# Performance work log

Hardware: AMD Instinct MI355X
Metric: run time of the kernel (lower is better)

The kernel has to match this reference:

```python
import jax, jax.numpy as jnp
import numpy as np

N = 50000      # nodes in batched graph
E = 800000     # directed edges
F_IN = 64      # node_feature_dim
F_E = 16       # edge_feature_dim
H = 4          # heads
C = 64         # hidden_dim per head
HC = H * C     # 256


def setup_inputs() -> dict:
    key = jax.random.key(0)
    ks = jax.random.split(key, 26)
    rn = lambda k, s, scale=0.1: jax.random.normal(k, s, dtype=jnp.float32) * scale
    inp = {}
    inp["x"] = rn(ks[0], (N, F_IN), 1.0)
    inp["edge_src"] = jax.random.randint(ks[1], (E,), 0, N)
    inp["edge_dst"] = jax.random.randint(ks[2], (E,), 0, N)
    inp["edge_attr"] = rn(ks[3], (E, F_E), 1.0)
    # GATConv layer 1 params
    inp["W1"] = rn(ks[4], (F_IN, HC))
    inp["atts1"] = rn(ks[5], (H, C))
    inp["attd1"] = rn(ks[6], (H, C))
    inp["We1"] = rn(ks[7], (F_E, HC))
    inp["atte1"] = rn(ks[8], (H, C))
    inp["b1"] = jnp.zeros((HC,), jnp.float32)
    inp["g1"] = jnp.ones((HC,), jnp.float32)
    inp["be1"] = jnp.zeros((HC,), jnp.float32)
    # GATConv layer 2 params
    inp["W2"] = rn(ks[9], (HC, HC))
    inp["atts2"] = rn(ks[10], (H, C))
    inp["attd2"] = rn(ks[11], (H, C))
    inp["We2"] = rn(ks[12], (F_E, HC))
    inp["atte2"] = rn(ks[13], (H, C))
    inp["b2"] = jnp.zeros((HC,), jnp.float32)
    inp["g2"] = jnp.ones((HC,), jnp.float32)
    inp["be2"] = jnp.zeros((HC,), jnp.float32)
    # output head
    inp["Wout"] = rn(ks[14], (HC, 1))
    inp["bout"] = jnp.zeros((1,), jnp.float32)
    return inp


def _gat_layer(x, src, dst, eattr, W, att_s, att_d, We, att_e, b):
    """PyG GATConv (concat=True, add_self_loops with fill_value='mean', eval so no dropout)."""
    n = x.shape[0]
    e = src.shape[0]
    # self-loop edge attr = mean of incoming edge attrs per node (0 if none)
    deg = jax.ops.segment_sum(jnp.ones((e,), x.dtype), dst, num_segments=n)
    loop_attr = jax.ops.segment_sum(eattr, dst, num_segments=n) / jnp.maximum(deg, 1.0)[:, None]
    loop = jnp.arange(n)
    src2 = jnp.concatenate([src, loop])
    dst2 = jnp.concatenate([dst, loop])
    ea2 = jnp.concatenate([eattr, loop_attr], axis=0)
    xs = (x @ W).reshape(n, H, C)                          # [N,H,C]
    a_s = jnp.einsum('nhc,hc->nh', xs, att_s)              # [N,H]
    a_d = jnp.einsum('nhc,hc->nh', xs, att_d)
    ee = (ea2 @ We).reshape(-1, H, C)                      # [E+N,H,C]
    a_e = jnp.einsum('ehc,hc->eh', ee, att_e)
    logits = jax.nn.leaky_relu(a_s[src2] + a_d[dst2] + a_e, 0.2)  # [E+N,H]
    m = jax.ops.segment_max(logits, dst2, num_segments=n)
    p = jnp.exp(logits - m[dst2])
    denom = jax.ops.segment_sum(p, dst2, num_segments=n)[dst2] + 1e-16
    alpha = p / denom                                      # segment softmax per dst node
    out = jax.ops.segment_sum(xs[src2] * alpha[:, :, None], dst2, num_segments=n)
    return out.reshape(n, HC) + b


def _bn_relu(x, g, b):
    # BatchNorm1d in training mode (batch statistics), eps=1e-5
    mu = x.mean(axis=0)
    var = ((x - mu) ** 2).mean(axis=0)
    return jax.nn.relu(g * (x - mu) * jax.lax.rsqrt(var + 1e-5) + b)


def reference(x, edge_src, edge_dst, edge_attr,
              W1, atts1, attd1, We1, atte1, b1, g1, be1,
              W2, atts2, attd2, We2, atte2, b2, g2, be2,
              Wout, bout):
    h = _gat_layer(x, edge_src, edge_dst, edge_attr, W1, atts1, attd1, We1, atte1, b1)
    h = _bn_relu(h, g1, be1)
    h = _gat_layer(h, edge_src, edge_dst, edge_attr, W2, atts2, attd2, We2, atte2, b2)
    h = _bn_relu(h, g2, be2)
    return h @ Wout + bout
```

## Files before the change

kernel.cpp:

```cpp
#include <hip/hip_runtime.h>
#include <hip/hip_bf16.h>
#include <stdint.h>

#define NNODES 50000
#define NEDGES 800000
#define HC 256

typedef unsigned short u16;
typedef __attribute__((ext_vector_type(8))) short bf16x8;
typedef __attribute__((ext_vector_type(4))) float f32x4;

__device__ __forceinline__ float b2f(u16 v) {
    return __uint_as_float(((unsigned)v) << 16);
}
__device__ __forceinline__ u16 f2b(float f) {
    unsigned u = __float_as_uint(f);
    u += 0x7fff + ((u >> 16) & 1);
    return (u16)(u >> 16);
}

__device__ __constant__ int dPO[19] = {0,16384,16640,16896,20992,21248,21504,21760,22016,
                                       87552,87808,88064,92160,92416,92672,92928,93184,93440,93441};
static const int hPO[19] = {0,16384,16640,16896,20992,21248,21504,21760,22016,
                            87552,87808,88064,92160,92416,92672,92928,93184,93440,93441};
#define TOTP 93441

__global__ void zero_init(unsigned* __restrict__ p, long nwords) {
    long i = (long)blockIdx.x * blockDim.x + threadIdx.x;
    long stride = (long)gridDim.x * blockDim.x;
    for (; i < nwords; i += stride) p[i] = 0u;
}

__global__ void detect_dtype(const unsigned* __restrict__ xbits, int* __restrict__ flag) {
    __shared__ int cnt;
    if (threadIdx.x == 0) cnt = 0;
    __syncthreads();
    int sane = 0;
    for (int i = threadIdx.x; i < 1024; i += 256) {
        unsigned lo = xbits[i] & 0xffffu;
        int e = (int)((lo >> 7) & 0xff);
        if (e >= 117 && e <= 133) sane++;
    }
    atomicAdd(&cnt, sane);
    __syncthreads();
    if (threadIdx.x == 0) *flag = (cnt >= 512) ? 1 : 0;
}

__global__ void cvt_bf16(const void* __restrict__ src, u16* __restrict__ dst, int n,
                         const int* __restrict__ flag) {
    int isbf16 = *flag;
    int i = blockIdx.x * 256 + threadIdx.x;
    int stride = gridDim.x * 256;
    if (isbf16) {
        const u16* s = (const u16*)src;
        for (; i < n; i += stride) dst[i] = s[i];
    } else {
        const float* s = (const float*)src;
        for (; i < n; i += stride) dst[i] = f2b(s[i]);
    }
}

struct Ptrs18 { const void* s[18]; };
__global__ void cvt_params(Ptrs18 p, u16* __restrict__ dst, const int* __restrict__ flag) {
    int i = blockIdx.x * 256 + threadIdx.x;
    if (i >= TOTP) return;
    int isbf16 = *flag;
    int idx = 0;
    #pragma unroll
    for (int j = 1; j < 18; j++) idx += (i >= dPO[j]) ? 1 : 0;
    int rel = i - dPO[idx];
    dst[i] = isbf16 ? ((const u16*)p.s[idx])[rel] : f2b(((const float*)p.s[idx])[rel]);
}

__global__ void proj_weight(const u16* __restrict__ W, const u16* __restrict__ att,
                            float* __restrict__ out, int R) {
    int i = blockIdx.x * 256 + threadIdx.x;
    if (i >= R * 4) return;
    int f = i >> 2, h = i & 3;
    float s = 0.f;
    for (int c = 0; c < 64; c++)
        s += b2f(W[f * 256 + h * 64 + c]) * b2f(att[h * 64 + c]);
    out[i] = s;
}

__global__ void proj_weight2(const u16* __restrict__ W, const u16* __restrict__ atta,
                             const u16* __restrict__ attb,
                             float* __restrict__ outa, float* __restrict__ outb, int R) {
    int i = blockIdx.x * 256 + threadIdx.x;
    if (i >= R * 4) return;
    int f = i >> 2, h = i & 3;
    float sa = 0.f, sb = 0.f;
    for (int c = 0; c < 64; c++) {
        float w = b2f(W[f * 256 + h * 64 + c]);
        sa += w * b2f(atta[h * 64 + c]);
        sb += w * b2f(attb[h * 64 + c]);
    }
    outa[i] = sa;
    outb[i] = sb;
}

__global__ void transpose_w(const u16* __restrict__ W, u16* __restrict__ WT, int K) {
    int i = blockIdx.x * 256 + threadIdx.x;
    if (i >= K * 256) return;
    int k = i / 256, c = i % 256;
    WT[c * K + k] = W[i];
}

__global__ void edge_deg(const int* __restrict__ edst, int* __restrict__ deg) {
    int e = blockIdx.x * 256 + threadIdx.x;
    if (e >= NEDGES) return;
    atomicAdd(&deg[edst[e]], 1);
}

__global__ void block_sum(const int* __restrict__ deg, int* __restrict__ bsums, int n) {
    __shared__ int lds[256];
    int i = blockIdx.x * 256 + threadIdx.x;
    lds[threadIdx.x] = (i < n) ? deg[i] : 0;
    __syncthreads();
    for (int s = 128; s; s >>= 1) {
        if (threadIdx.x < s) lds[threadIdx.x] += lds[threadIdx.x + s];
        __syncthreads();
    }
    if (threadIdx.x == 0) bsums[blockIdx.x] = lds[0];
}

__global__ void scan_bsums(const int* __restrict__ bsums, int* __restrict__ boffs, int nb) {
    __shared__ int lds[256];
    int t = threadIdx.x;
    int v = (t < nb) ? bsums[t] : 0;
    lds[t] = v;
    __syncthreads();
    for (int s = 1; s < 256; s <<= 1) {
        int u = (t >= s) ? lds[t - s] : 0;
        __syncthreads();
        lds[t] += u;
        __syncthreads();
    }
    boffs[t] = lds[t] - v;
}

__global__ void write_offsets(const int* __restrict__ deg, const int* __restrict__ boffs,
                              int* __restrict__ off, int* __restrict__ cursor, int n) {
    __shared__ int lds[256];
    int t = threadIdx.x;
    int i = blockIdx.x * 256 + t;
    int v = (i < n) ? deg[i] : 0;
    lds[t] = v;
    __syncthreads();
    for (int s = 1; s < 256; s <<= 1) {
        int u = (t >= s) ? lds[t - s] : 0;
        __syncthreads();
        lds[t] += u;
        __syncthreads();
    }
    int exc = lds[t] - v + boffs[blockIdx.x];
    if (i < n) { off[i] = exc; cursor[i] = exc; }
}

__global__ __launch_bounds__(256) void edge_stage(
    const void* __restrict__ eattr_raw, const int* __restrict__ flag,
    const int* __restrict__ esrc, const int* __restrict__ edst,
    const float* __restrict__ ve1, const float* __restrict__ ve2,
    int* __restrict__ cursor, uint4* __restrict__ rec) {
    int e = blockIdx.x * 256 + threadIdx.x;
    if (e >= NEDGES) return;
    float a[16];
    if (*flag) {
        const u16* s = (const u16*)eattr_raw + (long)e * 16;
        const uint4* q = (const uint4*)s;
        uint4 q0 = q[0], q1 = q[1];
        unsigned w0[8] = {q0.x, q0.y, q0.z, q0.w, q1.x, q1.y, q1.z, q1.w};
        #pragma unroll
        for (int j = 0; j < 8; j++) {
            a[2 * j] = b2f((u16)(w0[j] & 0xffff));
            a[2 * j + 1] = b2f((u16)(w0[j] >> 16));
        }
    } else {
        const float* s = (const float*)eattr_raw + (long)e * 16;
        #pragma unroll
        for (int j = 0; j < 16; j += 4) {
            float4 q = *(const float4*)(s + j);
            a[j] = q.x; a[j + 1] = q.y; a[j + 2] = q.z; a[j + 3] = q.w;
        }
    }
    float s1[4], s2[4];
    #pragma unroll
    for (int h = 0; h < 4; h++) {
        float t1 = 0.f, t2 = 0.f;
        #pragma unroll
        for (int f = 0; f < 16; f++) {
            t1 += a[f] * ve1[f * 4 + h];
            t2 += a[f] * ve2[f * 4 + h];
        }
        s1[h] = t1;
        s2[h] = t2;
    }
    unsigned a1lo = (unsigned)f2b(s1[0]) | ((unsigned)f2b(s1[1]) << 16);
    unsigned a1hi = (unsigned)f2b(s1[2]) | ((unsigned)f2b(s1[3]) << 16);
    unsigned a2lo = (unsigned)f2b(s2[0]) | ((unsigned)f2b(s2[1]) << 16);
    unsigned a2hi = (unsigned)f2b(s2[2]) | ((unsigned)f2b(s2[3]) << 16);
    int d = edst[e];
    int p = atomicAdd(&cursor[d], 1);
    unsigned src = (unsigned)esrc[e];
    rec[(long)p * 2 + 0] = make_uint4(src, a1lo, a1hi, 0u);
    rec[(long)p * 2 + 1] = make_uint4(src, a2lo, a2hi, 0u);
}

__global__ void bn_coef(const float* __restrict__ stats, const u16* __restrict__ g,
                        const u16* __restrict__ be, float* __restrict__ coef) {
    int c = threadIdx.x;
    float mu = stats[c] * (1.0f / NNODES);
    float var = stats[256 + c] * (1.0f / NNODES) - mu * mu;
    var = fmaxf(var, 0.f);
    float rs = rsqrtf(var + 1e-5f);
    float sc = b2f(g[c]) * rs;
    coef[c] = sc;
    coef[256 + c] = b2f(be[c]) - sc * mu;
}

template <int K, bool BN>
__global__ __launch_bounds__(256) void gemm_mfma(const u16* __restrict__ A,
                                                 const u16* __restrict__ WT,
                                                 const float* __restrict__ coef,
                                                 u16* __restrict__ out) {
    int tid = threadIdx.x;
    int wave = tid >> 6, lane = tid & 63;
    int quad = lane >> 4, l15 = lane & 15;
    long row0 = (long)blockIdx.x * 16;
    const u16* Arow = A + (row0 + l15) * K + quad * 8;
    const u16* Wbase = WT + (long)(wave * 64 + l15) * K + quad * 8;
    f32x4 acc[4] = {};
    for (int kk = 0; kk < K; kk += 32) {
        bf16x8 av = *(const bf16x8*)(Arow + kk);
        if (BN) {
            int kb = kk + quad * 8;
            float4 sc0 = *(const float4*)(coef + kb);
            float4 sc1 = *(const float4*)(coef + kb + 4);
            float4 sh0 = *(const float4*)(coef + 256 + kb);
            float4 sh1 = *(const float4*)(coef + 256 + kb + 4);
            float scl[8] = {sc0.x, sc0.y, sc0.z, sc0.w, sc1.x, sc1.y, sc1.z, sc1.w};
            float shf[8] = {sh0.x, sh0.y, sh0.z, sh0.w, sh1.x, sh1.y, sh1.z, sh1.w};
            #pragma unroll
            for (int j = 0; j < 8; j++) {
                float v = b2f((u16)av[j]);
                v = fmaxf(v * scl[j] + shf[j], 0.f);
                av[j] = (short)f2b(v);
            }
        }
        #pragma unroll
        for (int nt = 0; nt < 4; nt++) {
            bf16x8 bv = *(const bf16x8*)(Wbase + (long)nt * 16 * K + kk);
            acc[nt] = __builtin_amdgcn_mfma_f32_16x16x32_bf16(av, bv, acc[nt], 0, 0, 0);
        }
    }
    u16* orow = out + row0 * HC;
    #pragma unroll
    for (int nt = 0; nt < 4; nt++) {
        #pragma unroll
        for (int j = 0; j < 4; j++) {
            int r = quad * 4 + j;
            int c = wave * 64 + nt * 16 + l15;
            orow[(long)r * HC + c] = f2b(acc[nt][j]);
        }
    }
}

template <int K, bool BN>
__global__ __launch_bounds__(256) void proj_att(const u16* __restrict__ X,
                                                const float* __restrict__ coef,
                                                const float* __restrict__ us,
                                                const float* __restrict__ ud,
                                                float* __restrict__ as_, float* __restrict__ ad_) {
    int wid = (blockIdx.x * 256 + threadIdx.x) >> 6;
    int lane = threadIdx.x & 63;
    if (wid >= NNODES) return;
    float pas[4] = {0.f, 0.f, 0.f, 0.f}, pad[4] = {0.f, 0.f, 0.f, 0.f};
    const u16* row = X + (long)wid * K;
    for (int f = lane; f < K; f += 64) {
        float xv = b2f(row[f]);
        if (BN) xv = fmaxf(xv * coef[f] + coef[256 + f], 0.f);
        #pragma unroll
        for (int h = 0; h < 4; h++) {
            pas[h] += xv * us[f * 4 + h];
            pad[h] += xv * ud[f * 4 + h];
        }
    }
    #pragma unroll
    for (int h = 0; h < 4; h++) {
        for (int o = 32; o; o >>= 1) {
            pas[h] += __shfl_down(pas[h], o);
            pad[h] += __shfl_down(pad[h], o);
        }
    }
    if (lane == 0) {
        #pragma unroll
        for (int h = 0; h < 4; h++) {
            as_[wid * 4 + h] = pas[h];
            ad_[wid * 4 + h] = pad[h];
        }
    }
}

__global__ __launch_bounds__(256) void gat_fused(
    const u16* __restrict__ xs, const float* __restrict__ as_, const float* __restrict__ ad_,
    const uint4* __restrict__ rec, int layer,
    const int* __restrict__ off, const int* __restrict__ deg,
    const u16* __restrict__ bias, u16* __restrict__ out) {
    __shared__ int s_lds[4][64];
    __shared__ float w_lds[4][64][4];
    int wid = (blockIdx.x * 256 + threadIdx.x) >> 6;
    if (wid >= NNODES) return;
    int wave = threadIdx.x >> 6;
    int lane = threadIdx.x & 63;
    int d = wid;
    int st = off[d], dg = deg[d];
    int slot = lane >> 2, h = lane & 3;
    float adv = ad_[d * 4 + h];
    float m = -1e30f, s = 0.f, sae = 0.f;
    const uint4* rbase = rec + (long)st * 2 + layer;

    if (dg <= 64) {
        for (int i = slot; i < dg; i += 16) {
            uint4 r4 = rbase[(long)i * 2];
            int src = (int)r4.x;
            unsigned wsel = (h & 2) ? r4.z : r4.y;
            float aev = b2f((u16)((h & 1) ? (wsel >> 16) : (wsel & 0xffffu)));
            float t = as_[src * 4 + h] + adv + aev;
            float lg = (t > 0.f) ? t : 0.2f * t;
            if (h == 0) s_lds[wave][i] = src;
            w_lds[wave][i][h] = lg;
            sae += aev;
            float mn = fmaxf(m, lg);
            s = s * __expf(m - mn) + __expf(lg - mn);
            m = mn;
        }
        #pragma unroll
        for (int o = 4; o < 64; o <<= 1) {
            float mo = __shfl_xor(m, o), so = __shfl_xor(s, o), ao = __shfl_xor(sae, o);
            float mn = fmaxf(m, mo);
            s = s * __expf(m - mn) + so * __expf(mo - mn);
            m = mn;
            sae += ao;
        }
        float invs, wself;
        {
            float asv = as_[d * 4 + h];
            float l0 = asv + adv + sae / fmaxf((float)dg, 1.f);
            l0 = (l0 > 0.f) ? l0 : 0.2f * l0;
            float mn = fmaxf(m, l0);
            s = s * __expf(m - mn) + __expf(l0 - mn);
            m = mn;
            invs = 1.f / s;
            wself = __expf(l0 - mn) * invs;
        }
        for (int i = slot; i < dg; i += 16)
            w_lds[wave][i][h] = __expf(w_lds[wave][i][h] - m) * invs;

        int cg = lane & 31, half = lane >> 5;
        int ch8 = cg * 8;
        int h2 = cg >> 3;
        float ws2 = __shfl(wself, h2);
        const u16* xbase = xs + ch8;
        float a0, a1, a2, a3, a4, a5, a6, a7;
        {
            uint4 v = *(const uint4*)(xbase + (long)d * HC);
            float wsf = half ? 0.f : ws2;
            a0 = wsf * b2f((u16)(v.x & 0xffffu)); a1 = wsf * b2f((u16)(v.x >> 16));
            a2 = wsf * b2f((u16)(v.y & 0xffffu)); a3 = wsf * b2f((u16)(v.y >> 16));
            a4 = wsf * b2f((u16)(v.z & 0xffffu)); a5 = wsf * b2f((u16)(v.z >> 16));
            a6 = wsf * b2f((u16)(v.w & 0xffffu)); a7 = wsf * b2f((u16)(v.w >> 16));
        }
        int i = half;
        for (; i + 6 < dg; i += 8) {
            float wA = w_lds[wave][i][h2];     int sA = s_lds[wave][i];
            float wB = w_lds[wave][i + 2][h2]; int sB = s_lds[wave][i + 2];
            float wC = w_lds[wave][i + 4][h2]; int sC = s_lds[wave][i + 4];
            float wD = w_lds[wave][i + 6][h2]; int sD = s_lds[wave][i + 6];
            uint4 vA = *(const uint4*)(xbase + (long)sA * HC);
            uint4 vB = *(const uint4*)(xbase + (long)sB * HC);
            uint4 vC = *(const uint4*)(xbase + (long)sC * HC);
            uint4 vD = *(const uint4*)(xbase + (long)sD * HC);
            a0 += wA * b2f((u16)(vA.x & 0xffffu)) + wB * b2f((u16)(vB.x & 0xffffu))
                + wC * b2f((u16)(vC.x & 0xffffu)) + wD * b2f((u16)(vD.x & 0xffffu));
            a1 += wA * b2f((u16)(vA.x >> 16))     + wB * b2f((u16)(vB.x >> 16))
                + wC * b2f((u16)(vC.x >> 16))     + wD * b2f((u16)(vD.x >> 16));
            a2 += wA * b2f((u16)(vA.y & 0xffffu)) + wB * b2f((u16)(vB.y & 0xffffu))
                + wC * b2f((u16)(vC.y & 0xffffu)) + wD * b2f((u16)(vD.y & 0xffffu));
            a3 += wA * b2f((u16)(vA.y >> 16))     + wB * b2f((u16)(vB.y >> 16))
                + wC * b2f((u16)(vC.y >> 16))     + wD * b2f((u16)(vD.y >> 16));
            a4 += wA * b2f((u16)(vA.z & 0xffffu)) + wB * b2f((u16)(vB.z & 0xffffu))
                + wC * b2f((u16)(vC.z & 0xffffu)) + wD * b2f((u16)(vD.z & 0xffffu));
            a5 += wA * b2f((u16)(vA.z >> 16))     + wB * b2f((u16)(vB.z >> 16))
                + wC * b2f((u16)(vC.z >> 16))     + wD * b2f((u16)(vD.z >> 16));
            a6 += wA * b2f((u16)(vA.w & 0xffffu)) + wB * b2f((u16)(vB.w & 0xffffu))
                + wC * b2f((u16)(vC.w & 0xffffu)) + wD * b2f((u16)(vD.w & 0xffffu));
            a7 += wA * b2f((u16)(vA.w >> 16))     + wB * b2f((u16)(vB.w >> 16))
                + wC * b2f((u16)(vC.w >> 16))     + wD * b2f((u16)(vD.w >> 16));
        }
        for (; i < dg; i += 2) {
            float wA = w_lds[wave][i][h2]; int sA = s_lds[wave][i];
            uint4 vA = *(const uint4*)(xbase + (long)sA * HC);
            a0 += wA * b2f((u16)(vA.x & 0xffffu)); a1 += wA * b2f((u16)(vA.x >> 16));
            a2 += wA * b2f((u16)(vA.y & 0xffffu)); a3 += wA * b2f((u16)(vA.y >> 16));
            a4 += wA * b2f((u16)(vA.z & 0xffffu)); a5 += wA * b2f((u16)(vA.z >> 16));
            a6 += wA * b2f((u16)(vA.w & 0xffffu)); a7 += wA * b2f((u16)(vA.w >> 16));
        }
        a0 += __shfl_xor(a0, 32); a1 += __shfl_xor(a1, 32);
        a2 += __shfl_xor(a2, 32); a3 += __shfl_xor(a3, 32);
        a4 += __shfl_xor(a4, 32); a5 += __shfl_xor(a5, 32);
        a6 += __shfl_xor(a6, 32); a7 += __shfl_xor(a7, 32);
        if (half == 0) {
            uint4 bv = *(const uint4*)(bias + ch8);
            a0 += b2f((u16)(bv.x & 0xffffu)); a1 += b2f((u16)(bv.x >> 16));
            a2 += b2f((u16)(bv.y & 0xffffu)); a3 += b2f((u16)(bv.y >> 16));
            a4 += b2f((u16)(bv.z & 0xffffu)); a5 += b2f((u16)(bv.z >> 16));
            a6 += b2f((u16)(bv.w & 0xffffu)); a7 += b2f((u16)(bv.w >> 16));
            uint4 ov;
            ov.x = (unsigned)f2b(a0) | ((unsigned)f2b(a1) << 16);
            ov.y = (unsigned)f2b(a2) | ((unsigned)f2b(a3) << 16);
            ov.z = (unsigned)f2b(a4) | ((unsigned)f2b(a5) << 16);
            ov.w = (unsigned)f2b(a6) | ((unsigned)f2b(a7) << 16);
            *(uint4*)(out + (long)d * HC + ch8) = ov;
        }
        return;
    }

    for (int base = 0; base < dg; base += 16) {
        int i = base + slot;
        float lg = -1e30f, aev = 0.f, w = 0.f;
        if (i < dg) {
            uint4 r4 = rbase[(long)i * 2];
            int src = (int)r4.x;
            unsigned wsel = (h & 2) ? r4.z : r4.y;
            aev = b2f((u16)((h & 1) ? (wsel >> 16) : (wsel & 0xffffu)));
            float t = as_[src * 4 + h] + adv + aev;
            lg = (t > 0.f) ? t : 0.2f * t;
        }
        sae += aev;
        float mn = fmaxf(m, lg);
        if (i < dg) w = __expf(lg - mn);
        s = s * __expf(m - mn) + w;
        m = mn;
    }
    #pragma unroll
    for (int o = 4; o < 64; o <<= 1) {
        float mo = __shfl_xor(m, o), so = __shfl_xor(s, o), ao = __shfl_xor(sae, o);
        float mn = fmaxf(m, mo);
        s = s * __expf(m - mn) + so * __expf(mo - mn);
        m = mn;
        sae += ao;
    }
    float invs, wself;
    {
        float asv = as_[d * 4 + h];
        float l0 = asv + adv + sae / fmaxf((float)dg, 1.f);
        l0 = (l0 > 0.f) ? l0 : 0.2f * l0;
        float mn = fmaxf(m, l0);
        s = s * __expf(m - mn) + __expf(l0 - mn);
        m = mn;
        invs = 1.f / s;
        wself = __expf(l0 - mn) * invs;
    }
    int h2 = lane >> 4;
    float m2 = __shfl(m, h2);
    float is2 = __shfl(invs, h2);
    float ws2 = __shfl(wself, h2);
    float adv2 = __shfl(adv, h2);
    int cb = lane * 4;
    float a0, a1, a2, a3;
    {
        uint2 v = *(const uint2*)(xs + (long)d * HC + cb);
        a0 = ws2 * b2f((u16)(v.x & 0xffffu)); a1 = ws2 * b2f((u16)(v.x >> 16));
        a2 = ws2 * b2f((u16)(v.y & 0xffffu)); a3 = ws2 * b2f((u16)(v.y >> 16));
    }
    int slot16 = lane & 15;
    int lhi = lane & 48;
    for (int base = 0; base < dg; base += 16) {
        int cnt = min(16, dg - base);
        float wv = 0.f;
        int srcl = 0;
        if (slot16 < cnt) {
            uint4 r4 = rbase[(long)(base + slot16) * 2];
            srcl = (int)r4.x;
            unsigned wsel = (h2 & 2) ? r4.z : r4.y;
            float aev = b2f((u16)((h2 & 1) ? (wsel >> 16) : (wsel & 0xffffu)));
            float t = as_[srcl * 4 + h2] + adv2 + aev;
            t = (t > 0.f) ? t : 0.2f * t;
            wv = __expf(t - m2) * is2;
        }
        for (int j = 0; j < cnt; j++) {
            float w0 = __shfl(wv, lhi | j);
            int s0 = __shfl(srcl, j);
            uint2 v0 = *(const uint2*)(xs + (long)s0 * HC + cb);
            a0 += w0 * b2f((u16)(v0.x & 0xffffu));
            a1 += w0 * b2f((u16)(v0.x >> 16));
            a2 += w0 * b2f((u16)(v0.y & 0xffffu));
            a3 += w0 * b2f((u16)(v0.y >> 16));
        }
    }
    u16 o0 = f2b(a0 + b2f(bias[cb + 0]));
    u16 o1 = f2b(a1 + b2f(bias[cb + 1]));
    u16 o2 = f2b(a2 + b2f(bias[cb + 2]));
    u16 o3 = f2b(a3 + b2f(bias[cb + 3]));
    uint2 ov;
    ov.x = (unsigned)o0 | ((unsigned)o1 << 16);
    ov.y = (unsigned)o2 | ((unsigned)o3 << 16);
    *(uint2*)(out + (long)d * HC + cb) = ov;
}

__global__ void bn_stats(const u16* __restrict__ h, float* __restrict__ stats) {
    int c = threadIdx.x;
    float s = 0.f, q = 0.f;
    for (int r = blockIdx.x; r < NNODES; r += gridDim.x) {
        float v = b2f(h[(long)r * HC + c]);
        s += v;
        q += v * v;
    }
    atomicAdd(&stats[c], s);
    atomicAdd(&stats[256 + c], q);
}

__global__ __launch_bounds__(256) void out_head(const u16* __restrict__ h,
                                                const float* __restrict__ coef,
                                                const u16* __restrict__ wout,
                                                const u16* __restrict__ bout,
                                                void* __restrict__ y,
                                                const int* __restrict__ flag) {
    int wid = (blockIdx.x * 256 + threadIdx.x) >> 6;
    int lane = threadIdx.x & 63;
    if (wid >= NNODES) return;
    const u16* r = h + (long)wid * HC + lane * 4;
    int c0 = lane * 4;
    float p = 0.f;
    #pragma unroll
    for (int j = 0; j < 4; j++) {
        float v = b2f(r[j]);
        v = fmaxf(v * coef[c0 + j] + coef[256 + c0 + j], 0.f);
        p += v * b2f(wout[c0 + j]);
    }
    for (int o = 32; o; o >>= 1) p += __shfl_down(p, o);
    if (lane == 0) {
        float v = p + b2f(bout[0]);
        if (*flag) ((u16*)y)[wid] = f2b(v);
        else       ((float*)y)[wid] = v;
    }
}

extern "C" void kernel_launch(void* const* d_in, const int* in_sizes, int n_in,
                              void* d_out, int out_size, void* d_ws, size_t ws_size,
                              hipStream_t stream) {
    (void)in_sizes; (void)n_in; (void)out_size; (void)ws_size;
    const void* x_raw     = d_in[0];
    const int*  esrc      = (const int*)d_in[1];
    const int*  edst      = (const int*)d_in[2];
    const void* eattr_raw = d_in[3];

    char* ws = (char*)d_ws;
    size_t o = 0;
    auto alloc = [&](size_t bytes) -> char* {
        o = (o + 255) & ~(size_t)255;
        char* p = ws + o;
        o += bytes;
        return p;
    };
    int* dflag = (int*)alloc(256);
    u16* xb   = (u16*)alloc((size_t)NNODES * 64 * 2);
    u16* pall = (u16*)alloc((size_t)TOTP * 2);
    u16 *W1b = pall + hPO[0], *atts1b = pall + hPO[1], *attd1b = pall + hPO[2],
        *We1b = pall + hPO[3], *atte1b = pall + hPO[4], *b1b = pall + hPO[5],
        *g1b = pall + hPO[6], *be1b = pall + hPO[7], *W2b = pall + hPO[8],
        *atts2b = pall + hPO[9], *attd2b = pall + hPO[10], *We2b = pall + hPO[11],
        *atte2b = pall + hPO[12], *b2b = pall + hPO[13], *g2b = pall + hPO[14],
        *be2b = pall + hPO[15], *Woutb = pall + hPO[16], *boutb = pall + hPO[17];
    u16* WT1 = (u16*)alloc(256 * 64 * 2);
    u16* WT2 = (u16*)alloc(256 * 256 * 2);
    float* ve1 = (float*)alloc(64 * 4);
    float* ve2 = (float*)alloc(64 * 4);
    float* us1 = (float*)alloc(256 * 4);
    float* ud1 = (float*)alloc(256 * 4);
    float* us2 = (float*)alloc(1024 * 4);
    float* ud2 = (float*)alloc(1024 * 4);
    float* coef1 = (float*)alloc(512 * 4);
    float* coef2 = (float*)alloc(512 * 4);
    int* deg = (int*)alloc((size_t)NNODES * 4);
    float* stats1 = (float*)alloc(512 * 4);
    float* stats2 = (float*)alloc(512 * 4);
    size_t zero_end = o;
    size_t zero_begin = (size_t)((char*)deg - ws);
    int* off = (int*)alloc((size_t)NNODES * 4);
    int* cursor = (int*)alloc((size_t)NNODES * 4);
    int* bsums = (int*)alloc(256 * 4);
    int* boffs = (int*)alloc(256 * 4);
    uint4* rec = (uint4*)alloc((size_t)NEDGES * 32);
    float* as_ = (float*)alloc((size_t)NNODES * 16);
    float* ad_ = (float*)alloc((size_t)NNODES * 16);
    u16* bufA = (u16*)alloc((size_t)NNODES * HC * 2);
    u16* bufB = (u16*)alloc((size_t)NNODES * HC * 2);

    long zwords = (long)((zero_end - zero_begin) / 4);
    zero_init<<<128, 256, 0, stream>>>((unsigned*)(ws + zero_begin), zwords);
    detect_dtype<<<1, 256, 0, stream>>>((const unsigned*)x_raw, dflag);

    cvt_bf16<<<2048, 256, 0, stream>>>(x_raw, xb, NNODES * 64, dflag);
    Ptrs18 pp;
    for (int i = 0; i < 18; i++) pp.s[i] = d_in[4 + i];
    cvt_params<<<(TOTP + 255) / 256, 256, 0, stream>>>(pp, pall, dflag);

    transpose_w<<<64, 256, 0, stream>>>(W1b, WT1, 64);
    transpose_w<<<256, 256, 0, stream>>>(W2b, WT2, 256);
    proj_weight<<<1, 256, 0, stream>>>(We1b, atte1b, ve1, 16);
    proj_weight<<<1, 256, 0, stream>>>(We2b, atte2b, ve2, 16);
    proj_weight2<<<1, 256, 0, stream>>>(W1b, atts1b, attd1b, us1, ud1, 64);
    proj_weight2<<<4, 256, 0, stream>>>(W2b, atts2b, attd2b, us2, ud2, 256);

    int eblocks = (NEDGES + 255) / 256;
    int nb = (NNODES + 255) / 256;
    edge_deg<<<eblocks, 256, 0, stream>>>(edst, deg);
    block_sum<<<nb, 256, 0, stream>>>(deg, bsums, NNODES);
    scan_bsums<<<1, 256, 0, stream>>>(bsums, boffs, nb);
    write_offsets<<<nb, 256, 0, stream>>>(deg, boffs, off, cursor, NNODES);
    edge_stage<<<eblocks, 256, 0, stream>>>(eattr_raw, dflag, esrc, edst, ve1, ve2,
                                            cursor, rec);

    int mtiles = NNODES / 16;
    int wblocks = (NNODES * 64 + 255) / 256;

    gemm_mfma<64, false><<<mtiles, 256, 0, stream>>>(xb, WT1, nullptr, bufA);
    proj_att<64, false><<<wblocks, 256, 0, stream>>>(xb, nullptr, us1, ud1, as_, ad_);
    gat_fused<<<wblocks, 256, 0, stream>>>(bufA, as_, ad_, rec, 0, off, deg, b1b, bufB);
    bn_stats<<<512, 256, 0, stream>>>(bufB, stats1);
    bn_coef<<<1, 256, 0, stream>>>(stats1, g1b, be1b, coef1);

    gemm_mfma<256, true><<<mtiles, 256, 0, stream>>>(bufB, WT2, coef1, bufA);
    proj_att<256, true><<<wblocks, 256, 0, stream>>>(bufB, coef1, us2, ud2, as_, ad_);
    gat_fused<<<wblocks, 256, 0, stream>>>(bufA, as_, ad_, rec, 1, off, deg, b2b, bufB);
    bn_stats<<<512, 256, 0, stream>>>(bufB, stats2);
    bn_coef<<<1, 256, 0, stream>>>(stats2, g2b, be2b, coef2);

    out_head<<<wblocks, 256, 0, stream>>>(bufB, coef2, Woutb, boutb, d_out, dflag);
}
```

Baseline: 617.5 us.

## Use LDS-tiled 128x128 MFMA GEMM and split BN-ReLU into separate in-place pass

```diff
diff --git a/kernel.cpp b/kernel.cpp
--- a/kernel.cpp
+++ b/kernel.cpp
@@ -218,49 +218,89 @@
     coef[256 + c] = b2f(be[c]) - sc * mu;
 }
 
-template <int K, bool BN>
-__global__ __launch_bounds__(256) void gemm_mfma(const u16* __restrict__ A,
+__global__ __launch_bounds__(256) void bn_apply(u16* __restrict__ h,
+                                                const float* __restrict__ coef) {
+    long i = (long)blockIdx.x * 256 + threadIdx.x;
+    long total = (long)NNODES * (HC / 8);
+    long stride = (long)gridDim.x * 256;
+    int cpos = (int)(i & 31) * 8;
+    float scl[8], shf[8];
+    #pragma unroll
+    for (int j = 0; j < 8; j++) {
+        scl[j] = coef[cpos + j];
+        shf[j] = coef[256 + cpos + j];
+    }
+    for (; i < total; i += stride) {
+        uint4 v = *((const uint4*)h + i);
+        unsigned w[4] = {v.x, v.y, v.z, v.w};
+        #pragma unroll
+        for (int q = 0; q < 4; q++) {
+            float lo = b2f((u16)(w[q] & 0xffffu));
+            float hi = b2f((u16)(w[q] >> 16));
+            lo = fmaxf(lo * scl[2 * q] + shf[2 * q], 0.f);
+            hi = fmaxf(hi * scl[2 * q + 1] + shf[2 * q + 1], 0.f);
+            w[q] = (unsigned)f2b(lo) | ((unsigned)f2b(hi) << 16);
+        }
+        *((uint4*)h + i) = make_uint4(w[0], w[1], w[2], w[3]);
+    }
+}
+
+__device__ __forceinline__ void gload_lds16(const u16* g, u16* l) {
+    __builtin_amdgcn_global_load_lds(
+        (const __attribute__((address_space(1))) unsigned*)g,
+        (__attribute__((address_space(3))) unsigned*)l, 16, 0, 0);
+}
+
+template <int K>
+__global__ __launch_bounds__(256) void gemm_tile(const u16* __restrict__ A,
                                                  const u16* __restrict__ WT,
-                                                 const float* __restrict__ coef,
                                                  u16* __restrict__ out) {
+    __shared__ u16 As[128 * 32];
+    __shared__ u16 Bs[128 * 32];
     int tid = threadIdx.x;
     int wave = tid >> 6, lane = tid & 63;
+    int wr = wave >> 1, wc = wave & 1;
     int quad = lane >> 4, l15 = lane & 15;
-    long row0 = (long)blockIdx.x * 16;
-    const u16* Arow = A + (row0 + l15) * K + quad * 8;
-    const u16* Wbase = WT + (long)(wave * 64 + l15) * K + quad * 8;
-    f32x4 acc[4] = {};
+    long row0 = (long)(blockIdx.x >> 1) * 128;
+    int col0 = (blockIdx.x & 1) * 128;
+    int srow = lane >> 2;
+    int soct = (lane & 3) * 8;
+    f32x4 acc[4][4] = {};
     for (int kk = 0; kk < K; kk += 32) {
-        bf16x8 av = *(const bf16x8*)(Arow + kk);
-        if (BN) {
-            int kb = kk + quad * 8;
-            float4 sc0 = *(const float4*)(coef + kb);
-            float4 sc1 = *(const float4*)(coef + kb + 4);
-            float4 sh0 = *(const float4*)(coef + 256 + kb);
-            float4 sh1 = *(const float4*)(coef + 256 + kb + 4);
-            float scl[8] = {sc0.x, sc0.y, sc0.z, sc0.w, sc1.x, sc1.y, sc1.z, sc1.w};
-            float shf[8] = {sh0.x, sh0.y, sh0.z, sh0.w, sh1.x, sh1.y, sh1.z, sh1.w};
+        #pragma unroll
+        for (int sub = 0; sub < 2; sub++) {
+            int rr = wave * 32 + sub * 16;
+            long gr = row0 + rr + srow;
+            if (gr >= NNODES) gr = NNODES - 1;
+            gload_lds16(A + gr * K + kk + soct, &As[rr * 32]);
+            gload_lds16(WT + (long)(col0 + rr + srow) * K + kk + soct, &Bs[rr * 32]);
+        }
+        __syncthreads();
+        bf16x8 av[4], bv[4];
+        #pragma unroll
+        for (int m = 0; m < 4; m++)
+            av[m] = *(const bf16x8*)&As[(wr * 64 + m * 16 + l15) * 32 + quad * 8];
+        #pragma unroll
+        for (int n = 0; n < 4; n++)
+            bv[n] = *(const bf16x8*)&Bs[(wc * 64 + n * 16 + l15) * 32 + quad * 8];
+        #pragma unroll
+        for (int m = 0; m < 4; m++)
             #pragma unroll
-            for (int j = 0; j < 8; j++) {
-                float v = b2f((u16)av[j]);
-                v = fmaxf(v * scl[j] + shf[j], 0.f);
-                av[j] = (short)f2b(v);
+            for (int n = 0; n < 4; n++)
+                acc[m][n] = __builtin_amdgcn_mfma_f32_16x16x32_bf16(av[m], bv[n],
+                                                                    acc[m][n], 0, 0, 0);
+        __syncthreads();
+    }
+    #pragma unroll
+    for (int m = 0; m < 4; m++) {
+        #pragma unroll
+        for (int j = 0; j < 4; j++) {
+            long r = row0 + wr * 64 + m * 16 + quad * 4 + j;
+            if (r < NNODES) {
+                u16* op = out + r * HC + col0 + wc * 64 + l15;
+                #pragma unroll
+                for (int n = 0; n < 4; n++) op[n * 16] = f2b(acc[m][n][j]);
             }
-        }
-        #pragma unroll
-        for (int nt = 0; nt < 4; nt++) {
-            bf16x8 bv = *(const bf16x8*)(Wbase + (long)nt * 16 * K + kk);
-            acc[nt] = __builtin_amdgcn_mfma_f32_16x16x32_bf16(av, bv, acc[nt], 0, 0, 0);
-        }
-    }
-    u16* orow = out + row0 * HC;
-    #pragma unroll
-    for (int nt = 0; nt < 4; nt++) {
-        #pragma unroll
-        for (int j = 0; j < 4; j++) {
-            int r = quad * 4 + j;
-            int c = wave * 64 + nt * 16 + l15;
-            orow[(long)r * HC + c] = f2b(acc[nt][j]);
         }
     }
 }
@@ -622,17 +662,18 @@
     edge_stage<<<eblocks, 256, 0, stream>>>(eattr_raw, dflag, esrc, edst, ve1, ve2,
                                             cursor, rec);
 
-    int mtiles = NNODES / 16;
+    int gtiles = ((NNODES + 127) / 128) * 2;
     int wblocks = (NNODES * 64 + 255) / 256;
 
-    gemm_mfma<64, false><<<mtiles, 256, 0, stream>>>(xb, WT1, nullptr, bufA);
+    gemm_tile<64><<<gtiles, 256, 0, stream>>>(xb, WT1, bufA);
     proj_att<64, false><<<wblocks, 256, 0, stream>>>(xb, nullptr, us1, ud1, as_, ad_);
     gat_fused<<<wblocks, 256, 0, stream>>>(bufA, as_, ad_, rec, 0, off, deg, b1b, bufB);
     bn_stats<<<512, 256, 0, stream>>>(bufB, stats1);
     bn_coef<<<1, 256, 0, stream>>>(stats1, g1b, be1b, coef1);
 
-    gemm_mfma<256, true><<<mtiles, 256, 0, stream>>>(bufB, WT2, coef1, bufA);
-    proj_att<256, true><<<wblocks, 256, 0, stream>>>(bufB, coef1, us2, ud2, as_, ad_);
+    bn_apply<<<2048, 256, 0, stream>>>(bufB, coef1);
+    gemm_tile<256><<<gtiles, 256, 0, stream>>>(bufB, WT2, bufA);
+    proj_att<256, false><<<wblocks, 256, 0, stream>>>(bufB, nullptr, us2, ud2, as_, ad_);
     gat_fused<<<wblocks, 256, 0, stream>>>(bufA, as_, ad_, rec, 1, off, deg, b2b, bufB);
     bn_stats<<<512, 256, 0, stream>>>(bufB, stats2);
     bn_coef<<<1, 256, 0, stream>>>(stats2, g2b, be2b, coef2);
```

New measurement: 562.7 us. 1.1x faster.
